# Optimization experiments

Measured on AMD Instinct MI355X. Metric: run time of the kernel, lower is better.

Reference implementation:

```python
import jax, jax.numpy as jnp
import numpy as np

DIM = 1024
HEADS = 16
DIM_HEAD = 64
SCALE = DIM_HEAD ** -0.5


def setup_inputs() -> dict:
    key = jax.random.key(0)
    ks = jax.random.split(key, 7)
    init = lambda k, shape: jax.random.normal(k, shape, dtype=jnp.float32) * (shape[0] ** -0.5)
    return {
        "x": jax.random.normal(ks[0], (4, 4096, DIM), dtype=jnp.float32),
        "Wq": init(ks[1], (DIM, HEADS * DIM_HEAD)),
        "Wk": init(ks[2], (DIM, HEADS * DIM_HEAD)),
        "Wv": init(ks[3], (DIM, HEADS * DIM_HEAD)),
        "Wg": init(ks[4], (DIM, HEADS * DIM_HEAD)),
        "bg": jnp.zeros((HEADS * DIM_HEAD,), dtype=jnp.float32),
        "Wo": init(ks[5], (HEADS * DIM_HEAD, DIM)),
    }


def _split_heads(t):
    b, n, _ = t.shape
    return t.reshape(b, n, HEADS, DIM_HEAD).transpose(0, 2, 1, 3)  # b h n d


def reference(x, Wq, Wk, Wv, Wg, bg, Wo):
    # projections
    q = _split_heads(x @ Wq)
    k = _split_heads(x @ Wk)
    v = _split_heads(x @ Wv)
    g = _split_heads(x @ Wg + bg)

    # feature map + gate
    q = jax.nn.elu(q) + 1.0
    k = jax.nn.elu(k) + 1.0
    g = jax.nn.sigmoid(g)

    # linear attention: per-head kv state, no n x n scores
    kv = jnp.einsum("bhnd,bhne->bhde", k, v)          # [b,h,d,d]
    k_sum = k.sum(axis=-2)                              # [b,h,d]
    z = 1.0 / jnp.clip(jnp.einsum("bhnd,bhd->bhn", q, k_sum), 1e-6)
    out = jnp.einsum("bhnd,bhde->bhne", q * SCALE, kv)
    out = out * z[..., None] * g                        # [b,h,n,d]

    b, h, n, d = out.shape
    out = out.transpose(0, 2, 1, 3).reshape(b, n, h * d)
    return out @ Wo
```

## Files before the change

kernel.cpp:

```cpp
#include <hip/hip_runtime.h>
#include <math.h>

#define DIM 1024
#define SCALE 0.125f
#define NT 16

typedef __attribute__((ext_vector_type(8))) short bh8;
typedef __attribute__((ext_vector_type(4))) short bh4;
typedef __attribute__((ext_vector_type(4))) float f4v;

__device__ __forceinline__ unsigned short f2bf(float f) {
  unsigned u = __builtin_bit_cast(unsigned, f);
  return (unsigned short)((u + 0x7FFFu + ((u >> 16) & 1u)) >> 16);
}
__device__ __forceinline__ float bf2f(unsigned short u) {
  return __builtin_bit_cast(float, (unsigned)u << 16);
}
__device__ __forceinline__ float elu1(float v) {
  return v > 0.f ? v + 1.f : __expf(v);
}
__device__ __forceinline__ f4v mfma16(bh8 a, bh8 b, f4v c) {
  return __builtin_amdgcn_mfma_f32_16x16x32_bf16(a, b, c, 0, 0, 0);
}

typedef const void __attribute__((address_space(1)))* gas1_t;
typedef void __attribute__((address_space(3)))* las3_t;

__device__ __forceinline__ bh8 frag(const unsigned short* lds, int row, int k8) {
  const int q = ((row << 3) | k8) ^ (row & 7);
  return *reinterpret_cast<const bh8*>(lds + q * 8);
}

__device__ __forceinline__ void gll_tile(const unsigned short* g, int ldg,
                                         unsigned short* lds, int t) {
  const int lane = t & 63, w = t >> 6;
#pragma unroll
  for (int cc = 0; cc < 4; ++cc) {
    const int base = (w * 4 + cc) * 64;
    const int q = base + lane;
    const int c = q ^ ((q >> 3) & 7);
    __builtin_amdgcn_global_load_lds(
        (gas1_t)(const void*)(g + (size_t)(c >> 3) * ldg + (c & 7) * 8),
        (las3_t)(void*)(lds + (size_t)base * 8), 16, 0, 0);
  }
}

__global__ __launch_bounds__(256) void p0(const float* __restrict__ x,
                                          unsigned short* __restrict__ xb) {
  const size_t i = ((size_t)blockIdx.x * 256 + threadIdx.x) * 8;
  const float4 a = *reinterpret_cast<const float4*>(x + i);
  const float4 b = *reinterpret_cast<const float4*>(x + i + 4);
  bh8 v;
  v[0] = (short)f2bf(a.x); v[1] = (short)f2bf(a.y);
  v[2] = (short)f2bf(a.z); v[3] = (short)f2bf(a.w);
  v[4] = (short)f2bf(b.x); v[5] = (short)f2bf(b.y);
  v[6] = (short)f2bf(b.z); v[7] = (short)f2bf(b.w);
  *reinterpret_cast<bh8*>(xb + i) = v;
}

__global__ __launch_bounds__(256) void p1(
    const float* __restrict__ Wq, const float* __restrict__ Wk,
    const float* __restrict__ Wv, const float* __restrict__ Wg,
    const float* __restrict__ Wo, unsigned short* __restrict__ WallT,
    unsigned short* __restrict__ WoT) {
  const int m = blockIdx.z;
  const int tc = blockIdx.x, tr = blockIdx.y;
  const int t = threadIdx.x;
  const float* src = m == 0 ? Wq : m == 1 ? Wk : m == 2 ? Wv : m == 3 ? Wg : Wo;
  __shared__ float tile[64][65];
#pragma unroll
  for (int i = 0; i < 4; ++i) {
    const int idx = i * 256 + t;
    const int r = idx >> 4;
    const int c4 = (idx & 15) * 4;
    const float4 v = *reinterpret_cast<const float4*>(
        src + (size_t)(tr * 64 + r) * DIM + tc * 64 + c4);
    tile[r][c4] = v.x; tile[r][c4 + 1] = v.y;
    tile[r][c4 + 2] = v.z; tile[r][c4 + 3] = v.w;
  }
  __syncthreads();
  unsigned short* dst = (m < 4) ? WallT : WoT;
#pragma unroll
  for (int i = 0; i < 4; ++i) {
    const int idx = i * 256 + t;
    const int lc = idx >> 4;
    const int k4i = (idx & 15) * 4;
    const size_t drow = (m < 4) ? (size_t)(tc * 256 + m * 64 + lc)
                                : (size_t)(tc * 64 + lc);
    bh4 v;
#pragma unroll
    for (int jj = 0; jj < 4; ++jj) v[jj] = (short)f2bf(tile[k4i + jj][lc]);
    *reinterpret_cast<bh4*>(dst + drow * DIM + tr * 64 + k4i) = v;
  }
}

template <int MODE>
__global__ __launch_bounds__(512, 2) void gemm8(
    const unsigned short* __restrict__ gA,
    const unsigned short* __restrict__ gB, const float* __restrict__ bg,
    unsigned short* __restrict__ ob, float* __restrict__ of,
    float* __restrict__ kv_part, float* __restrict__ ksum_part) {
  const int t = threadIdx.x, lane = t & 63, w = t >> 6;
  const int wr = w >> 2, wc = w & 3, g4 = lane >> 4, c0 = lane & 15;
  const int nwg = gridDim.x;
  const int NBC = (MODE == 0) ? 16 : 4;
  const int rbn = nwg / NBC;
  const int bid = (int)blockIdx.x;
  const int xcd = bid & 7;
  const int idx = bid >> 3;
  const int bandsz = rbn >> 3;
  const int cb = idx / bandsz;
  const int rb = xcd * bandsz + (idx - cb * bandsz);

  constexpr int LDGA = (MODE == 0) ? 1024 : 4096;
  constexpr int ASTR = (MODE == 0) ? 64 : 256;
  constexpr int AOFF = (MODE == 0) ? 0 : 64;

  __shared__ __align__(16) unsigned short lds[65536];

  int offA[2], offB[2], dstc[2];
#pragma unroll
  for (int cc = 0; cc < 2; ++cc) {
    const int base = (w * 2 + cc) * 64;
    const int q = base + lane;
    const int c = q ^ ((q >> 3) & 7);
    offA[cc] = (c >> 3) * LDGA + (c & 7) * 8;
    offB[cc] = (c >> 3) * 1024 + (c & 7) * 8;
    dstc[cc] = base * 8;
  }
  const unsigned short* Abase = gA + (size_t)rb * 256 * LDGA + AOFF;
  const unsigned short* Bbase = gB + (size_t)cb * 256 * 1024;

#define SA(kt, half)                                                          \
  {                                                                           \
    _Pragma("unroll") for (int cc = 0; cc < 2; ++cc)                          \
        __builtin_amdgcn_global_load_lds(                                     \
            (gas1_t)(Abase + (size_t)(half) * 128 * LDGA + offA[cc] +         \
                     (kt) * ASTR),                                            \
            (las3_t)(lds + ((kt) & 1) * 16384 + (half) * 8192 + dstc[cc]),    \
            16, 0, 0);                                                        \
  }
#define SB(kt, half)                                                          \
  {                                                                           \
    _Pragma("unroll") for (int cc = 0; cc < 2; ++cc)                          \
        __builtin_amdgcn_global_load_lds(                                     \
            (gas1_t)(Bbase + (size_t)(half) * 128 * 1024 + offB[cc] +         \
                     (kt) * 64),                                              \
            (las3_t)(lds + 32768 + ((kt) & 1) * 16384 + (half) * 8192 +       \
                     dstc[cc]),                                               \
            16, 0, 0);                                                        \
  }

  f4v acc[8][4];
#pragma unroll
  for (int i = 0; i < 8; ++i)
#pragma unroll
    for (int j = 0; j < 4; ++j) acc[i][j] = (f4v){0.f, 0.f, 0.f, 0.f};

  SB(0, 0); SB(0, 1); SA(0, 0); SA(0, 1); SB(1, 0); SB(1, 1);

#pragma unroll 2
  for (int kt = 0; kt < NT; ++kt) {
    if (kt < NT - 1) {
      asm volatile("s_waitcnt vmcnt(4)" ::: "memory");
    } else {
      asm volatile("s_waitcnt vmcnt(0)" ::: "memory");
    }
    __builtin_amdgcn_sched_barrier(0);
    __builtin_amdgcn_s_barrier();
    const unsigned short* Ah = lds + (kt & 1) * 16384 + wr * 8192;
    const unsigned short* Bh =
        lds + 32768 + (kt & 1) * 16384 + (wc >> 1) * 8192;
    const int br0 = (wc & 1) * 64;

    bh8 bfr[4][2], a0[2][2];
#pragma unroll
    for (int nf = 0; nf < 4; ++nf)
#pragma unroll
      for (int kf = 0; kf < 2; ++kf)
        bfr[nf][kf] = frag(Bh, br0 + nf * 16 + c0, kf * 4 + g4);
#pragma unroll
    for (int i = 0; i < 2; ++i)
#pragma unroll
      for (int kf = 0; kf < 2; ++kf)
        a0[i][kf] = frag(Ah, i * 16 + c0, kf * 4 + g4);
    if (kt + 1 < NT) { SA(kt + 1, 0); SA(kt + 1, 1); }
    __builtin_amdgcn_s_barrier();
    __builtin_amdgcn_s_setprio(1);
#pragma unroll
    for (int i = 0; i < 2; ++i)
#pragma unroll
      for (int nf = 0; nf < 4; ++nf)
#pragma unroll
        for (int kf = 0; kf < 2; ++kf)
          acc[i][nf] = mfma16(bfr[nf][kf], a0[i][kf], acc[i][nf]);
    __builtin_amdgcn_s_setprio(0);
    __builtin_amdgcn_s_barrier();

    bh8 a1[2][2];
#pragma unroll
    for (int i = 0; i < 2; ++i)
#pragma unroll
      for (int kf = 0; kf < 2; ++kf)
        a1[i][kf] = frag(Ah, (2 + i) * 16 + c0, kf * 4 + g4);
    if (kt + 2 < NT) SB(kt + 2, 0);
    __builtin_amdgcn_s_barrier();
    __builtin_amdgcn_s_setprio(1);
#pragma unroll
    for (int i = 0; i < 2; ++i)
#pragma unroll
      for (int nf = 0; nf < 4; ++nf)
#pragma unroll
        for (int kf = 0; kf < 2; ++kf)
          acc[2 + i][nf] = mfma16(bfr[nf][kf], a1[i][kf], acc[2 + i][nf]);
    __builtin_amdgcn_s_setprio(0);
    __builtin_amdgcn_s_barrier();

    bh8 a2[2][2];
#pragma unroll
    for (int i = 0; i < 2; ++i)
#pragma unroll
      for (int kf = 0; kf < 2; ++kf)
        a2[i][kf] = frag(Ah, (4 + i) * 16 + c0, kf * 4 + g4);
    if (kt + 2 < NT) SB(kt + 2, 1);
    __builtin_amdgcn_s_barrier();
    __builtin_amdgcn_s_setprio(1);
#pragma unroll
    for (int i = 0; i < 2; ++i)
#pragma unroll
      for (int nf = 0; nf < 4; ++nf)
#pragma unroll
        for (int kf = 0; kf < 2; ++kf)
          acc[4 + i][nf] = mfma16(bfr[nf][kf], a2[i][kf], acc[4 + i][nf]);
    __builtin_amdgcn_s_setprio(0);
    __builtin_amdgcn_s_barrier();

    bh8 a3[2][2];
#pragma unroll
    for (int i = 0; i < 2; ++i)
#pragma unroll
      for (int kf = 0; kf < 2; ++kf)
        a3[i][kf] = frag(Ah, (6 + i) * 16 + c0, kf * 4 + g4);
    __builtin_amdgcn_s_barrier();
    __builtin_amdgcn_s_setprio(1);
#pragma unroll
    for (int i = 0; i < 2; ++i)
#pragma unroll
      for (int nf = 0; nf < 4; ++nf)
#pragma unroll
        for (int kf = 0; kf < 2; ++kf)
          acc[6 + i][nf] = mfma16(bfr[nf][kf], a3[i][kf], acc[6 + i][nf]);
    __builtin_amdgcn_s_setprio(0);
  }
#undef SA
#undef SB

  if (MODE == 0) {
    float bgv[4][4];
    if (wc == 3) {
#pragma unroll
      for (int nf = 0; nf < 4; ++nf) {
        const float4 bv =
            *reinterpret_cast<const float4*>(bg + cb * 64 + nf * 16 + g4 * 4);
        bgv[nf][0] = bv.x; bgv[nf][1] = bv.y;
        bgv[nf][2] = bv.z; bgv[nf][3] = bv.w;
      }
    }
#pragma unroll
    for (int rf = 0; rf < 8; ++rf) {
      const size_t row = (size_t)rb * 256 + wr * 128 + rf * 16 + c0;
#pragma unroll
      for (int nf = 0; nf < 4; ++nf) {
        ushort4 o;
#pragma unroll
        for (int r = 0; r < 4; ++r) {
          float v = acc[rf][nf][r];
          if (wc <= 1) v = elu1(v);
          else if (wc == 3) v = 1.f / (1.f + __expf(-(v + bgv[nf][r])));
          ((unsigned short*)&o)[r] = f2bf(v);
        }
        *reinterpret_cast<ushort4*>(
            ob + row * 4096 + cb * 256 + wc * 64 + nf * 16 + g4 * 4) = o;
      }
    }

    __syncthreads();
    if (wc == 1 || wc == 2) {
      unsigned short* dstT = lds + (wc == 2 ? 16896 : 0);
#pragma unroll
      for (int rf = 0; rf < 8; ++rf) {
        const int n = wr * 128 + rf * 16 + c0;
#pragma unroll
        for (int nf = 0; nf < 4; ++nf)
#pragma unroll
          for (int r = 0; r < 4; ++r) {
            float v = acc[rf][nf][r];
            if (wc == 1) v = elu1(v);
            dstT[(nf * 16 + g4 * 4 + r) * 264 + n] = f2bf(v);
          }
      }
    }
    __syncthreads();
    const unsigned short* kT = lds;
    const unsigned short* vT = lds + 16896;
    const size_t pbase = (size_t)((rb >> 4) * 16 + cb) * 16 + (rb & 15);
#pragma unroll
    for (int pi = 0; pi < 2; ++pi) {
      const int p = w * 2 + pi, dt = p >> 2, et = p & 3;
      f4v a = (f4v){0.f, 0.f, 0.f, 0.f};
#pragma unroll
      for (int kn = 0; kn < 8; ++kn) {
        const bh8 kq = *reinterpret_cast<const bh8*>(
            kT + (dt * 16 + c0) * 264 + kn * 32 + g4 * 8);
        const bh8 vq = *reinterpret_cast<const bh8*>(
            vT + (et * 16 + c0) * 264 + kn * 32 + g4 * 8);
        a = mfma16(vq, kq, a);
      }
      float4 o;
      o.x = a[0]; o.y = a[1]; o.z = a[2]; o.w = a[3];
      *reinterpret_cast<float4*>(
          kv_part + pbase * 4096 + (dt * 16 + c0) * 64 + et * 16 + g4 * 4) = o;
    }
    if (w < 4) {
      bh8 ones;
#pragma unroll
      for (int j = 0; j < 8; ++j) ones[j] = (short)0x3F80;
      f4v a = (f4v){0.f, 0.f, 0.f, 0.f};
#pragma unroll
      for (int kn = 0; kn < 8; ++kn) {
        const bh8 kq = *reinterpret_cast<const bh8*>(
            kT + (w * 16 + c0) * 264 + kn * 32 + g4 * 8);
        a = mfma16(ones, kq, a);
      }
      if (lane < 16) ksum_part[pbase * 64 + w * 16 + c0] = a[0];
    }
  } else {
#pragma unroll
    for (int rf = 0; rf < 8; ++rf) {
      const size_t row = (size_t)rb * 256 + wr * 128 + rf * 16 + c0;
#pragma unroll
      for (int nf = 0; nf < 4; ++nf) {
        float4 o;
        o.x = acc[rf][nf][0]; o.y = acc[rf][nf][1];
        o.z = acc[rf][nf][2]; o.w = acc[rf][nf][3];
        *reinterpret_cast<float4*>(
            of + row * DIM + cb * 256 + wc * 64 + nf * 16 + g4 * 4) = o;
      }
    }
  }
}

__global__ __launch_bounds__(256) void g2r(const float* __restrict__ kv_part,
                                           const float* __restrict__ ksum_part,
                                           unsigned short* __restrict__ kvT,
                                           float* __restrict__ ksum, int b0) {
  const int bhl = blockIdx.x, t = threadIdx.x;
  const size_t bh = (size_t)b0 * 16 + bhl;
#pragma unroll
  for (int i = 0; i < 16; ++i) {
    const int idx = i * 256 + t;
    const int d = idx >> 6, e = idx & 63;
    float s = 0.f;
    for (int sp = 0; sp < 16; ++sp)
      s += kv_part[((size_t)bhl * 16 + sp) * 4096 + idx];
    kvT[bh * 4096 + e * 64 + d] = f2bf(s);
  }
  if (t < 64) {
    float s = 0.f;
    for (int sp = 0; sp < 16; ++sp)
      s += ksum_part[((size_t)bhl * 16 + sp) * 64 + t];
    ksum[bh * 64 + t] = s;
  }
}

__global__ __launch_bounds__(256) void g3(unsigned short* __restrict__ qkvg,
                                          const unsigned short* __restrict__ kvT,
                                          const float* __restrict__ ksum,
                                          int b0) {
  const int h = blockIdx.x, z = blockIdx.y;
  const int t = threadIdx.x, lane = t & 63, w = t >> 6;
  const int g4 = lane >> 4, c0 = lane & 15;
  __shared__ unsigned short sQ[8192];
  __shared__ unsigned short skv[64 * 72];
  __shared__ float sks[64], sden[128];
  const int bb = z >> 5;
  const size_t bh = (size_t)(b0 + bb) * 16 + h;
  for (int i = t; i < 4096; i += 256)
    skv[(i >> 6) * 72 + (i & 63)] = kvT[bh * 4096 + i];
  if (t < 64) sks[t] = ksum[bh * 64 + t];
  const size_t row0 = (size_t)z * 128;
  gll_tile(qkvg + row0 * 4096 + h * 256, 4096, sQ, t);
  __syncthreads();
  {
    const int rr = t >> 1, hf = t & 1;
    float s = 0.f;
#pragma unroll
    for (int dd = 0; dd < 32; ++dd) {
      const int d = hf * 32 + dd;
      s += bf2f(sQ[(((rr << 3) | (d >> 3)) ^ (rr & 7)) * 8 + (d & 7)]) * sks[d];
    }
    s += __shfl_xor(s, 1, 64);
    if (hf == 0) sden[rr] = SCALE / fmaxf(s, 1e-6f);
  }
  __syncthreads();
  f4v oacc[2][4];
#pragma unroll
  for (int ii = 0; ii < 2; ++ii)
#pragma unroll
    for (int et = 0; et < 4; ++et) oacc[ii][et] = (f4v){0.f, 0.f, 0.f, 0.f};
#pragma unroll
  for (int kf = 0; kf < 2; ++kf) {
    bh8 aq[2];
#pragma unroll
    for (int ii = 0; ii < 2; ++ii)
      aq[ii] = frag(sQ, w * 32 + ii * 16 + c0, kf * 4 + g4);
#pragma unroll
    for (int et = 0; et < 4; ++et) {
      const bh8 bkv = *reinterpret_cast<const bh8*>(
          skv + (et * 16 + c0) * 72 + kf * 32 + g4 * 8);
#pragma unroll
      for (int ii = 0; ii < 2; ++ii)
        oacc[ii][et] = mfma16(bkv, aq[ii], oacc[ii][et]);
    }
  }
#pragma unroll
  for (int ii = 0; ii < 2; ++ii) {
    const int n = w * 32 + ii * 16 + c0;
    const float z2 = sden[n];
    const size_t rowbase = (row0 + n) * 4096 + h * 256;
#pragma unroll
    for (int et = 0; et < 4; ++et) {
      const ushort4 gt = *reinterpret_cast<const ushort4*>(
          qkvg + rowbase + 192 + et * 16 + g4 * 4);
      ushort4 o;
#pragma unroll
      for (int r = 0; r < 4; ++r)
        ((unsigned short*)&o)[r] =
            f2bf(oacc[ii][et][r] * z2 * bf2f(((const unsigned short*)&gt)[r]));
      *reinterpret_cast<ushort4*>(qkvg + rowbase + 64 + et * 16 + g4 * 4) = o;
    }
  }
}

extern "C" void kernel_launch(void* const* d_in, const int* in_sizes, int n_in,
                              void* d_out, int out_size, void* d_ws,
                              size_t ws_size, hipStream_t stream) {
  const float* x  = (const float*)d_in[0];
  const float* Wq = (const float*)d_in[1];
  const float* Wk = (const float*)d_in[2];
  const float* Wv = (const float*)d_in[3];
  const float* Wg = (const float*)d_in[4];
  const float* bg = (const float*)d_in[5];
  const float* Wo = (const float*)d_in[6];
  float* out = (float*)d_out;
  char* w = (char*)d_ws;

  const size_t PB = 46202880ull;
  int nbat = 1;
  if (ws_size >= 11026432ull + 4ull * PB) nbat = 4;
  else if (ws_size >= 11026432ull + 2ull * PB) nbat = 2;

  unsigned short* WallT = (unsigned short*)(w);
  unsigned short* WoT   = (unsigned short*)(w + 8388608);
  unsigned short* kvT   = (unsigned short*)(w + 10485760);
  float*          ksum  = (float*)(w + 11010048);
  char* dyn = w + 11026432;
  float* kv_part        = (float*)dyn;
  float* ksum_part      = (float*)(dyn + (size_t)nbat * 4194304);
  unsigned short* xb    = (unsigned short*)(dyn + (size_t)nbat * (4194304 + 65536));
  unsigned short* qkvg  = (unsigned short*)(dyn + (size_t)nbat * (4194304 + 65536 + 8388608));

  p1<<<dim3(16, 16, 5), 256, 0, stream>>>(Wq, Wk, Wv, Wg, Wo, WallT, WoT);

  for (int b0 = 0; b0 < 4; b0 += nbat) {
    const int rows_p = nbat * 4096;
    p0<<<rows_p / 2, 256, 0, stream>>>(x + (size_t)b0 * 4096 * DIM, xb);
    gemm8<0><<<dim3((rows_p / 256) * 16), 512, 0, stream>>>(
        xb, WallT, bg, qkvg, nullptr, kv_part, ksum_part);
    g2r<<<nbat * 16, 256, 0, stream>>>(kv_part, ksum_part, kvT, ksum, b0);
    g3<<<dim3(16, nbat * 32), 256, 0, stream>>>(qkvg, kvT, ksum, b0);
    gemm8<1><<<dim3((rows_p / 256) * 4), 512, 0, stream>>>(
        qkvg, WoT, nullptr, nullptr, out + (size_t)b0 * 4096 * DIM,
        nullptr, nullptr);
  }
}
```

Before: 296.7 us.

## Replace 8-phase GEMM pipeline with simple K=32 double-buffered loop

Rewrites the main GEMM loop to use K tiles of 32 instead of 64, a plain double buffer with one __syncthreads per iteration, and a new 4-chunk XOR swizzle. The old fine-grained phases with s_setprio, split barriers and staggered A/B prefetch are removed. LDS drops from 128KB to about 68KB, which could let more blocks fit per CU. The cost is twice as many iterations and barriers, and less overlap between memory loads and MFMA work.

```diff
diff --git a/kernel.cpp b/kernel.cpp
--- a/kernel.cpp
+++ b/kernel.cpp
@@ -3,7 +3,7 @@
 
 #define DIM 1024
 #define SCALE 0.125f
-#define NT 16
+#define NT2 32
 
 typedef __attribute__((ext_vector_type(8))) short bh8;
 typedef __attribute__((ext_vector_type(4))) short bh4;
@@ -26,11 +26,15 @@
 typedef const void __attribute__((address_space(1)))* gas1_t;
 typedef void __attribute__((address_space(3)))* las3_t;
 
+__device__ __forceinline__ bh8 frag2(const unsigned short* b, int row, int k8) {
+  const int q = (row << 2) | ((k8 ^ (row >> 1)) & 3);
+  return *reinterpret_cast<const bh8*>(b + q * 8);
+}
+
 __device__ __forceinline__ bh8 frag(const unsigned short* lds, int row, int k8) {
   const int q = ((row << 3) | k8) ^ (row & 7);
   return *reinterpret_cast<const bh8*>(lds + q * 8);
 }
-
 __device__ __forceinline__ void gll_tile(const unsigned short* g, int ldg,
                                          unsigned short* lds, int t) {
   const int lane = t & 63, w = t >> 6;
@@ -95,7 +99,7 @@
 }
 
 template <int MODE>
-__global__ __launch_bounds__(512, 2) void gemm8(
+__global__ __launch_bounds__(512, 2) void gemm97(
     const unsigned short* __restrict__ gA,
     const unsigned short* __restrict__ gB, const float* __restrict__ bg,
     unsigned short* __restrict__ ob, float* __restrict__ of,
@@ -113,42 +117,36 @@
   const int rb = xcd * bandsz + (idx - cb * bandsz);
 
   constexpr int LDGA = (MODE == 0) ? 1024 : 4096;
-  constexpr int ASTR = (MODE == 0) ? 64 : 256;
-  constexpr int AOFF = (MODE == 0) ? 0 : 64;
-
-  __shared__ __align__(16) unsigned short lds[65536];
+
+  __shared__ __align__(16) unsigned short lds[34816];
 
   int offA[2], offB[2], dstc[2];
 #pragma unroll
   for (int cc = 0; cc < 2; ++cc) {
-    const int base = (w * 2 + cc) * 64;
-    const int q = base + lane;
-    const int c = q ^ ((q >> 3) & 7);
-    offA[cc] = (c >> 3) * LDGA + (c & 7) * 8;
-    offB[cc] = (c >> 3) * 1024 + (c & 7) * 8;
-    dstc[cc] = base * 8;
-  }
-  const unsigned short* Abase = gA + (size_t)rb * 256 * LDGA + AOFF;
+    const int ch = (w * 2 + cc) * 64 + lane;
+    const int r_ = ch >> 2;
+    const int k8_ = (ch & 3) ^ ((r_ >> 1) & 3);
+    offA[cc] = r_ * LDGA + k8_ * 8;
+    offB[cc] = r_ * 1024 + k8_ * 8;
+    dstc[cc] = ch * 8;
+  }
+  const unsigned short* Abase = gA + (size_t)rb * 256 * LDGA;
   const unsigned short* Bbase = gB + (size_t)cb * 256 * 1024;
 
-#define SA(kt, half)                                                          \
+#define ACOFF(kt) ((MODE == 0) ? (kt) * 32 : (((kt) >> 1) * 256 + 64 + ((kt) & 1) * 32))
+#define SA2(kt, p)                                                            \
   {                                                                           \
     _Pragma("unroll") for (int cc = 0; cc < 2; ++cc)                          \
         __builtin_amdgcn_global_load_lds(                                     \
-            (gas1_t)(Abase + (size_t)(half) * 128 * LDGA + offA[cc] +         \
-                     (kt) * ASTR),                                            \
-            (las3_t)(lds + ((kt) & 1) * 16384 + (half) * 8192 + dstc[cc]),    \
-            16, 0, 0);                                                        \
-  }
-#define SB(kt, half)                                                          \
+            (gas1_t)(Abase + offA[cc] + ACOFF(kt)),                           \
+            (las3_t)(lds + (p) * 16384 + dstc[cc]), 16, 0, 0);                \
+  }
+#define SB2(kt, p)                                                            \
   {                                                                           \
     _Pragma("unroll") for (int cc = 0; cc < 2; ++cc)                          \
         __builtin_amdgcn_global_load_lds(                                     \
-            (gas1_t)(Bbase + (size_t)(half) * 128 * 1024 + offB[cc] +         \
-                     (kt) * 64),                                              \
-            (las3_t)(lds + 32768 + ((kt) & 1) * 16384 + (half) * 8192 +       \
-                     dstc[cc]),                                               \
-            16, 0, 0);                                                        \
+            (gas1_t)(Bbase + offB[cc] + (kt) * 32),                           \
+            (las3_t)(lds + (p) * 16384 + 8192 + dstc[cc]), 16, 0, 0);         \
   }
 
   f4v acc[8][4];
@@ -157,103 +155,31 @@
 #pragma unroll
     for (int j = 0; j < 4; ++j) acc[i][j] = (f4v){0.f, 0.f, 0.f, 0.f};
 
-  SB(0, 0); SB(0, 1); SA(0, 0); SA(0, 1); SB(1, 0); SB(1, 1);
+  SA2(0, 0); SB2(0, 0);
+  __syncthreads();
 
 #pragma unroll 2
-  for (int kt = 0; kt < NT; ++kt) {
-    if (kt < NT - 1) {
-      asm volatile("s_waitcnt vmcnt(4)" ::: "memory");
-    } else {
-      asm volatile("s_waitcnt vmcnt(0)" ::: "memory");
-    }
-    __builtin_amdgcn_sched_barrier(0);
-    __builtin_amdgcn_s_barrier();
-    const unsigned short* Ah = lds + (kt & 1) * 16384 + wr * 8192;
-    const unsigned short* Bh =
-        lds + 32768 + (kt & 1) * 16384 + (wc >> 1) * 8192;
-    const int br0 = (wc & 1) * 64;
-
-    bh8 bfr[4][2], a0[2][2];
+  for (int kt = 0; kt < NT2; ++kt) {
+    const int p = kt & 1;
+    if (kt + 1 < NT2) { SA2(kt + 1, p ^ 1); SB2(kt + 1, p ^ 1); }
+    const unsigned short* Ab = lds + p * 16384;
+    const unsigned short* Bb = Ab + 8192;
+    bh8 bq[4];
 #pragma unroll
     for (int nf = 0; nf < 4; ++nf)
-#pragma unroll
-      for (int kf = 0; kf < 2; ++kf)
-        bfr[nf][kf] = frag(Bh, br0 + nf * 16 + c0, kf * 4 + g4);
-#pragma unroll
-    for (int i = 0; i < 2; ++i)
-#pragma unroll
-      for (int kf = 0; kf < 2; ++kf)
-        a0[i][kf] = frag(Ah, i * 16 + c0, kf * 4 + g4);
-    if (kt + 1 < NT) { SA(kt + 1, 0); SA(kt + 1, 1); }
-    __builtin_amdgcn_s_barrier();
-    __builtin_amdgcn_s_setprio(1);
-#pragma unroll
-    for (int i = 0; i < 2; ++i)
+      bq[nf] = frag2(Bb, wc * 64 + nf * 16 + c0, g4);
+#pragma unroll
+    for (int rf = 0; rf < 8; ++rf) {
+      const bh8 aq = frag2(Ab, wr * 128 + rf * 16 + c0, g4);
 #pragma unroll
       for (int nf = 0; nf < 4; ++nf)
-#pragma unroll
-        for (int kf = 0; kf < 2; ++kf)
-          acc[i][nf] = mfma16(bfr[nf][kf], a0[i][kf], acc[i][nf]);
-    __builtin_amdgcn_s_setprio(0);
-    __builtin_amdgcn_s_barrier();
-
-    bh8 a1[2][2];
-#pragma unroll
-    for (int i = 0; i < 2; ++i)
-#pragma unroll
-      for (int kf = 0; kf < 2; ++kf)
-        a1[i][kf] = frag(Ah, (2 + i) * 16 + c0, kf * 4 + g4);
-    if (kt + 2 < NT) SB(kt + 2, 0);
-    __builtin_amdgcn_s_barrier();
-    __builtin_amdgcn_s_setprio(1);
-#pragma unroll
-    for (int i = 0; i < 2; ++i)
-#pragma unroll
-      for (int nf = 0; nf < 4; ++nf)
-#pragma unroll
-        for (int kf = 0; kf < 2; ++kf)
-          acc[2 + i][nf] = mfma16(bfr[nf][kf], a1[i][kf], acc[2 + i][nf]);
-    __builtin_amdgcn_s_setprio(0);
-    __builtin_amdgcn_s_barrier();
-
-    bh8 a2[2][2];
-#pragma unroll
-    for (int i = 0; i < 2; ++i)
-#pragma unroll
-      for (int kf = 0; kf < 2; ++kf)
-        a2[i][kf] = frag(Ah, (4 + i) * 16 + c0, kf * 4 + g4);
-    if (kt + 2 < NT) SB(kt + 2, 1);
-    __builtin_amdgcn_s_barrier();
-    __builtin_amdgcn_s_setprio(1);
-#pragma unroll
-    for (int i = 0; i < 2; ++i)
-#pragma unroll
-      for (int nf = 0; nf < 4; ++nf)
-#pragma unroll
-        for (int kf = 0; kf < 2; ++kf)
-          acc[4 + i][nf] = mfma16(bfr[nf][kf], a2[i][kf], acc[4 + i][nf]);
-    __builtin_amdgcn_s_setprio(0);
-    __builtin_amdgcn_s_barrier();
-
-    bh8 a3[2][2];
-#pragma unroll
-    for (int i = 0; i < 2; ++i)
-#pragma unroll
-      for (int kf = 0; kf < 2; ++kf)
-        a3[i][kf] = frag(Ah, (6 + i) * 16 + c0, kf * 4 + g4);
-    __builtin_amdgcn_s_barrier();
-    __builtin_amdgcn_s_setprio(1);
-#pragma unroll
-    for (int i = 0; i < 2; ++i)
-#pragma unroll
-      for (int nf = 0; nf < 4; ++nf)
-#pragma unroll
-        for (int kf = 0; kf < 2; ++kf)
-          acc[6 + i][nf] = mfma16(bfr[nf][kf], a3[i][kf], acc[6 + i][nf]);
-    __builtin_amdgcn_s_setprio(0);
-  }
-#undef SA
-#undef SB
+        acc[rf][nf] = mfma16(bq[nf], aq, acc[rf][nf]);
+    }
+    __syncthreads();
+  }
+#undef SA2
+#undef SB2
+#undef ACOFF
 
   if (MODE == 0) {
     float bgv[4][4];
@@ -284,9 +210,10 @@
       }
     }
 
+    asm volatile("s_waitcnt vmcnt(0)" ::: "memory");
     __syncthreads();
     if (wc == 1 || wc == 2) {
-      unsigned short* dstT = lds + (wc == 2 ? 16896 : 0);
+      unsigned short* dstT = lds + (wc == 2 ? 16640 : 0);
 #pragma unroll
       for (int rf = 0; rf < 8; ++rf) {
         const int n = wr * 128 + rf * 16 + c0;
@@ -296,13 +223,13 @@
           for (int r = 0; r < 4; ++r) {
             float v = acc[rf][nf][r];
             if (wc == 1) v = elu1(v);
-            dstT[(nf * 16 + g4 * 4 + r) * 264 + n] = f2bf(v);
+            dstT[(nf * 16 + g4 * 4 + r) * 260 + n] = f2bf(v);
           }
       }
     }
     __syncthreads();
     const unsigned short* kT = lds;
-    const unsigned short* vT = lds + 16896;
+    const unsigned short* vT = lds + 16640;
     const size_t pbase = (size_t)((rb >> 4) * 16 + cb) * 16 + (rb & 15);
 #pragma unroll
     for (int pi = 0; pi < 2; ++pi) {
@@ -311,9 +238,9 @@
 #pragma unroll
       for (int kn = 0; kn < 8; ++kn) {
         const bh8 kq = *reinterpret_cast<const bh8*>(
-            kT + (dt * 16 + c0) * 264 + kn * 32 + g4 * 8);
+            kT + (dt * 16 + c0) * 260 + kn * 32 + g4 * 8);
         const bh8 vq = *reinterpret_cast<const bh8*>(
-            vT + (et * 16 + c0) * 264 + kn * 32 + g4 * 8);
+            vT + (et * 16 + c0) * 260 + kn * 32 + g4 * 8);
         a = mfma16(vq, kq, a);
       }
       float4 o;
@@ -329,7 +256,7 @@
 #pragma unroll
       for (int kn = 0; kn < 8; ++kn) {
         const bh8 kq = *reinterpret_cast<const bh8*>(
-            kT + (w * 16 + c0) * 264 + kn * 32 + g4 * 8);
+            kT + (w * 16 + c0) * 260 + kn * 32 + g4 * 8);
         a = mfma16(ones, kq, a);
       }
       if (lane < 16) ksum_part[pbase * 64 + w * 16 + c0] = a[0];
@@ -475,11 +402,11 @@
   for (int b0 = 0; b0 < 4; b0 += nbat) {
     const int rows_p = nbat * 4096;
     p0<<<rows_p / 2, 256, 0, stream>>>(x + (size_t)b0 * 4096 * DIM, xb);
-    gemm8<0><<<dim3((rows_p / 256) * 16), 512, 0, stream>>>(
+    gemm97<0><<<dim3((rows_p / 256) * 16), 512, 0, stream>>>(
         xb, WallT, bg, qkvg, nullptr, kv_part, ksum_part);
     g2r<<<nbat * 16, 256, 0, stream>>>(kv_part, ksum_part, kvT, ksum, b0);
     g3<<<dim3(16, nbat * 32), 256, 0, stream>>>(qkvg, kvT, ksum, b0);
-    gemm8<1><<<dim3((rows_p / 256) * 4), 512, 0, stream>>>(
+    gemm97<1><<<dim3((rows_p / 256) * 4), 512, 0, stream>>>(
         qkvg, WoT, nullptr, nullptr, out + (size_t)b0 * 4096 * DIM,
         nullptr, nullptr);
   }
```

After: 320.8 us. 1.08x slower.
